# Kernel optimization log

Measured on AMD Instinct MI355X. Metric: run time of the kernel, lower is better.

The kernel has to match this reference:

```python
import jax, jax.numpy as jnp
import numpy as np

N = 100000
E = 1600000
D_IN = 128
D_HID = 128
D_OUT = 64


def mish(x):
    return x * jnp.tanh(jax.nn.softplus(x))


def sage_conv(x, src, dst, W_l, b_l, W_r):
    # gather source-node features along edges, mean-aggregate at destination
    msg = x[src]  # [E, d]
    agg = jax.ops.segment_sum(msg, dst, num_segments=N)  # [N, d]
    cnt = jax.ops.segment_sum(jnp.ones((E,), x.dtype), dst, num_segments=N)
    agg = agg / jnp.maximum(cnt, 1.0)[:, None]
    # PyG SAGEConv: lin_l(aggregated) + lin_r(root); lin_r has no bias
    return agg @ W_l.T + b_l + x @ W_r.T


def setup_inputs() -> dict:
    key = jax.random.key(0)
    ks = jax.random.split(key, 10)
    s = lambda d: 1.0 / np.sqrt(d)
    return {
        "x": jax.random.normal(ks[0], (N, D_IN), jnp.float32),
        "edge_index": jax.random.randint(ks[1], (2, E), 0, N, jnp.int64),
        "W_l0": jax.random.normal(ks[2], (D_HID, D_IN), jnp.float32) * s(D_IN),
        "b_l0": jnp.zeros((D_HID,), jnp.float32),
        "W_r0": jax.random.normal(ks[3], (D_HID, D_IN), jnp.float32) * s(D_IN),
        "W_l1": jax.random.normal(ks[4], (D_HID, D_HID), jnp.float32) * s(D_HID),
        "b_l1": jnp.zeros((D_HID,), jnp.float32),
        "W_r1": jax.random.normal(ks[5], (D_HID, D_HID), jnp.float32) * s(D_HID),
        "W_head": jax.random.normal(ks[6], (D_OUT, D_HID), jnp.float32) * s(D_HID),
        "b_head": jnp.zeros((D_OUT,), jnp.float32),
    }


def reference(x, edge_index, W_l0, b_l0, W_r0, W_l1, b_l1, W_r1, W_head, b_head):
    src, dst = edge_index[0], edge_index[1]
    h = mish(sage_conv(x, src, dst, W_l0, b_l0, W_r0))  # dropout is identity in eval
    h = mish(sage_conv(h, src, dst, W_l1, b_l1, W_r1))
    return h @ W_head.T + b_head
```

## Files before the change

### kernel.cpp

```cpp
#include <hip/hip_runtime.h>
#include <math.h>

#define N_NODES 100000
#define N_EDGES 1600000
#define DF      128
#define D_HEAD  64

#define NWIN    128
#define WIN_SZ  782
#define CAP     13312
#define BCH     8192

typedef __attribute__((ext_vector_type(8))) short bf16x8;
typedef __attribute__((ext_vector_type(4))) float f32x4;

static __device__ __forceinline__ float mish_f(float v) {
    float e = __expf(v);
    float q = 1.0f + e;
    float p = q * q;
    float m = v * (p - 1.0f) / (p + 1.0f);
    return (v > 40.0f) ? v : m;
}

static __device__ __forceinline__ unsigned short f2bf(float f) {
    unsigned int u = __builtin_bit_cast(unsigned int, f);
    unsigned int r = (u + 0x7fffu + ((u >> 16) & 1u)) >> 16;
    return (unsigned short)r;
}


#define XB 12500
#define WB 288

__global__ void cvt_kernel(const float* __restrict__ x,
                           const float* __restrict__ Wl0, const float* __restrict__ Wr0,
                           const float* __restrict__ Wl1, const float* __restrict__ Wr1,
                           const float* __restrict__ Wh,
                           unsigned short* __restrict__ xb, unsigned short* __restrict__ wb,
                           int* __restrict__ bucket_cnt) {
    int b = blockIdx.x;
    if (b < XB) {
        int i = b * 256 + threadIdx.x;
        float4 v = ((const float4*)x)[i];
        ushort4 o;
        o.x = f2bf(v.x); o.y = f2bf(v.y); o.z = f2bf(v.z); o.w = f2bf(v.w);
        ((ushort4*)xb)[i] = o;
    } else if (b < XB + WB) {
        int id = (b - XB) * 256 + threadIdx.x;
        if (id < 65536) {
            int seg = id >> 14;
            int r   = id & 16383;
            const float* W = (seg == 0) ? Wl0 : (seg == 1) ? Wr0 : (seg == 2) ? Wl1 : Wr1;
            wb[id] = f2bf(W[r]);
        } else {
            wb[id] = f2bf(Wh[id - 65536]);
        }
    } else {
        if (threadIdx.x < NWIN) bucket_cnt[threadIdx.x] = 0;
    }
}


__global__ __launch_bounds__(256) void bucket_kernel(const int* __restrict__ src,
                                                     const int* __restrict__ dst,
                                                     int* __restrict__ bucket_cnt,
                                                     unsigned int* __restrict__ pairs) {
    __shared__ int cnt[NWIN][4];
    __shared__ int cur[NWIN][4];
    int tid = threadIdx.x;
    int set = tid & 3;
    int e0  = blockIdx.x * BCH;
    for (int i = tid; i < NWIN * 4; i += 256) ((int*)cnt)[i] = 0;
    __syncthreads();

    int dc[BCH / 256];
    #pragma unroll 4
    for (int i = 0; i < BCH / 256; ++i) {
        int e = e0 + tid + i * 256;
        int d = (e < N_EDGES) ? dst[e] : -1;
        dc[i] = d;
        if (d >= 0) atomicAdd(&cnt[d / WIN_SZ][set], 1);
    }
    __syncthreads();
    if (tid < NWIN) {
        int c0 = cnt[tid][0], c1 = cnt[tid][1], c2 = cnt[tid][2], c3 = cnt[tid][3];
        int b = atomicAdd(&bucket_cnt[tid], c0 + c1 + c2 + c3);
        cur[tid][0] = b;
        cur[tid][1] = b + c0;
        cur[tid][2] = b + c0 + c1;
        cur[tid][3] = b + c0 + c1 + c2;
    }
    __syncthreads();
    #pragma unroll 4
    for (int i = 0; i < BCH / 256; ++i) {
        int d = dc[i];
        if (d >= 0) {
            int e  = e0 + tid + i * 256;
            int s  = src[e];
            int w  = d / WIN_SZ;
            int dl = d - w * WIN_SZ;
            int idx = atomicAdd(&cur[w][set], 1);
            if (idx < CAP)
                pairs[(size_t)w * CAP + idx] = (unsigned)s | ((unsigned)dl << 17);
        }
    }
}


__global__ __launch_bounds__(256) void build_win(const unsigned int* __restrict__ pairs,
                                                 const int* __restrict__ bucket_cnt,
                                                 int* __restrict__ rowstart,
                                                 int* __restrict__ csr) {
    __shared__ int ldeg[WIN_SZ];
    __shared__ int lcsr[CAP];
    __shared__ int wsum[4];
    __shared__ int red[4];

    int tid = threadIdx.x;
    int w   = blockIdx.x;
    int base_node = w * WIN_SZ;
    int nn = N_NODES - base_node;
    if (nn > WIN_SZ) nn = WIN_SZ;
    if (nn < 0) nn = 0;

    for (int i = tid; i < WIN_SZ; i += 256) ldeg[i] = 0;

    int val = (tid < w) ? bucket_cnt[tid] : 0;
    #pragma unroll
    for (int o = 32; o; o >>= 1) val += __shfl_xor(val, o);
    if ((tid & 63) == 0) red[tid >> 6] = val;
    int n_pairs = bucket_cnt[w];
    if (n_pairs > CAP) n_pairs = CAP;
    __syncthreads();
    int ebase = red[0] + red[1] + red[2] + red[3];

    const unsigned int* pw = pairs + (size_t)w * CAP;

    for (int i = tid; i < n_pairs; i += 256)
        atomicAdd(&ldeg[pw[i] >> 17], 1);
    __syncthreads();

    int i0 = tid * 4;
    int v[4];
    int s = 0;
    #pragma unroll
    for (int q = 0; q < 4; ++q) {
        v[q] = (i0 + q < nn) ? ldeg[i0 + q] : 0;
        s += v[q];
    }
    int lane = tid & 63, wv = tid >> 6;
    int sc = s;
    #pragma unroll
    for (int d = 1; d < 64; d <<= 1) {
        int t = __shfl_up(sc, d);
        if (lane >= d) sc += t;
    }
    if (lane == 63) wsum[wv] = sc;
    __syncthreads();
    int woff = 0;
    for (int q = 0; q < wv; ++q) woff += wsum[q];
    int run = woff + sc - s;
    #pragma unroll
    for (int q = 0; q < 4; ++q) {
        if (i0 + q < nn) {
            rowstart[base_node + i0 + q] = ebase + run;
            ldeg[i0 + q] = run;
            run += v[q];
        }
    }
    if (w == NWIN - 1 && tid == 0) rowstart[N_NODES] = N_EDGES;
    __syncthreads();

    for (int i = tid; i < n_pairs; i += 256) {
        unsigned int p = pw[i];
        int slot = atomicAdd(&ldeg[p >> 17], 1);
        lcsr[slot] = (int)(p & 0x1FFFFu);
    }
    __syncthreads();

    for (int i = tid; i < n_pairs; i += 256)
        csr[ebase + i] = lcsr[i];
}


__global__ __launch_bounds__(256) void aggregate_kernel(const unsigned short* __restrict__ X,
                                                        const int* __restrict__ rowstart,
                                                        const int* __restrict__ csr,
                                                        unsigned short* __restrict__ out) {
    int wv   = threadIdx.x >> 6;
    int lane = threadIdx.x & 63;
    int node = blockIdx.x * 4 + wv;
    if (node >= N_NODES) return;
    int slot = lane >> 4;
    int l16  = lane & 15;
    int rs0 = rowstart[node];
    int rs1 = rowstart[node + 1];

    float acc[8];
    #pragma unroll
    for (int i = 0; i < 8; ++i) acc[i] = 0.f;

    for (int e0 = rs0; e0 < rs1; e0 += 16) {
        uint4 v[4];
        #pragma unroll
        for (int j = 0; j < 4; ++j) {
            int e = e0 + 4 * j + slot;
            uint4 t = {0u, 0u, 0u, 0u};
            if (e < rs1) t = *(const uint4*)(X + (size_t)csr[e] * DF + l16 * 8);
            v[j] = t;
        }
        #pragma unroll
        for (int j = 0; j < 4; ++j) {
            unsigned int w0[4] = {v[j].x, v[j].y, v[j].z, v[j].w};
            #pragma unroll
            for (int i = 0; i < 4; ++i) {
                acc[2 * i]     += __builtin_bit_cast(float, w0[i] << 16);
                acc[2 * i + 1] += __builtin_bit_cast(float, w0[i] & 0xffff0000u);
            }
        }
    }

    #pragma unroll
    for (int i = 0; i < 8; ++i) {
        acc[i] += __shfl_xor(acc[i], 32);
        acc[i] += __shfl_xor(acc[i], 16);
    }

    int d = rs1 - rs0;
    float inv = 1.0f / (float)(d > 0 ? d : 1);
    if (slot == 0) {
        unsigned int r[4];
        #pragma unroll
        for (int i = 0; i < 4; ++i) {
            unsigned int lo = f2bf(acc[2 * i] * inv);
            unsigned int hi = f2bf(acc[2 * i + 1] * inv);
            r[i] = lo | (hi << 16);
        }
        uint4 o = {r[0], r[1], r[2], r[3]};
        *(uint4*)(out + (size_t)node * DF + l16 * 8) = o;
    }
}


template <int COLS, bool TWO, bool MISH, bool OUT_BF16>
__global__ __launch_bounds__(256, 3) void sage_gemm(const unsigned short* __restrict__ A,
                                                    const unsigned short* __restrict__ H,
                                                    const unsigned short* __restrict__ Wl,
                                                    const unsigned short* __restrict__ Wr,
                                                    const float* __restrict__ bias,
                                                    void* __restrict__ out) {
    constexpr int NT  = COLS / 16;
    constexpr int LDA = 136;
    __shared__ unsigned short Ws[COLS * LDA];

    int tid  = threadIdx.x;
    int wv   = tid >> 6;
    int lane = tid & 63;
    int quad = lane >> 4;
    int l16  = lane & 15;
    int m0   = blockIdx.x * 128;

    int arow0 = m0 + wv * 32 + l16;
    int arow1 = arow0 + 16;
    if (arow0 > N_NODES - 1) arow0 = N_NODES - 1;
    if (arow1 > N_NODES - 1) arow1 = N_NODES - 1;

    f32x4 acc[2][NT];
    #pragma unroll
    for (int t = 0; t < 2; ++t)
        #pragma unroll
        for (int n = 0; n < NT; ++n) acc[t][n] = (f32x4){0.f, 0.f, 0.f, 0.f};

    #pragma unroll
    for (int phase = 0; phase < (TWO ? 2 : 1); ++phase) {
        const unsigned short* Ain = phase ? H : A;
        const unsigned short* Win = phase ? Wr : Wl;
        if (phase) __syncthreads();
        #pragma unroll
        for (int i = 0; i < COLS / 16; ++i) {
            int idx = tid + i * 256;
            int r   = idx >> 4;
            int cb  = (idx & 15) * 8;
            *(uint4*)&Ws[r * LDA + cb] = *(const uint4*)&Win[r * 128 + cb];
        }
        __syncthreads();

        const unsigned short* Ap0 = Ain + (size_t)arow0 * 128 + quad * 8;
        const unsigned short* Ap1 = Ain + (size_t)arow1 * 128 + quad * 8;
        #pragma unroll
        for (int ks = 0; ks < 4; ++ks) {
            bf16x8 af0 = *(const bf16x8*)(Ap0 + ks * 32);
            bf16x8 af1 = *(const bf16x8*)(Ap1 + ks * 32);
            #pragma unroll
            for (int n = 0; n < NT; ++n) {
                bf16x8 bfr = *(const bf16x8*)&Ws[(n * 16 + l16) * LDA + ks * 32 + quad * 8];
                acc[0][n] = __builtin_amdgcn_mfma_f32_16x16x32_bf16(af0, bfr, acc[0][n], 0, 0, 0);
                acc[1][n] = __builtin_amdgcn_mfma_f32_16x16x32_bf16(af1, bfr, acc[1][n], 0, 0, 0);
            }
        }
    }

    #pragma unroll
    for (int t = 0; t < 2; ++t) {
        #pragma unroll
        for (int n = 0; n < NT; ++n) {
            int col = n * 16 + l16;
            float b = bias[col];
            #pragma unroll
            for (int r = 0; r < 4; ++r) {
                int row = m0 + wv * 32 + t * 16 + quad * 4 + r;
                if (row < N_NODES) {
                    float v = acc[t][n][r] + b;
                    if constexpr (MISH) v = mish_f(v);
                    if constexpr (OUT_BF16)
                        ((unsigned short*)out)[(size_t)row * COLS + col] = f2bf(v);
                    else
                        ((float*)out)[(size_t)row * COLS + col] = v;
                }
            }
        }
    }
}


extern "C" void kernel_launch(void* const* d_in, const int* in_sizes, int n_in,
                              void* d_out, int out_size, void* d_ws, size_t ws_size,
                              hipStream_t stream) {
    const float* x   = (const float*)d_in[0];
    const int*   ei  = (const int*)d_in[1];
    const float* Wl0 = (const float*)d_in[2];
    const float* bl0 = (const float*)d_in[3];
    const float* Wr0 = (const float*)d_in[4];
    const float* Wl1 = (const float*)d_in[5];
    const float* bl1 = (const float*)d_in[6];
    const float* Wr1 = (const float*)d_in[7];
    const float* Wh  = (const float*)d_in[8];
    const float* bh  = (const float*)d_in[9];
    float* out = (float*)d_out;

    const int* src = ei;
    const int* dst = ei + N_EDGES;

    char* ws = (char*)d_ws;
    size_t off = 0;
    auto alloc = [&](size_t bytes) -> void* {
        void* p = ws + off;
        off += (bytes + 255) & ~(size_t)255;
        return p;
    };
    int* rowstart   = (int*)alloc((N_NODES + 1) * 4);
    int* csr        = (int*)alloc(N_EDGES * 4);
    int* bucket_cnt = (int*)alloc(NWIN * 4);

    unsigned short* Wb  = (unsigned short*)alloc((size_t)(65536 + 8192) * 2);
    unsigned short* Xb  = (unsigned short*)alloc((size_t)N_NODES * DF * 2);
    unsigned short* Ab  = (unsigned short*)alloc((size_t)N_NODES * DF * 2);
    unsigned short* H1b = (unsigned short*)alloc((size_t)N_NODES * DF * 2);

    unsigned short* Wlb0 = Wb;
    unsigned short* Wrb0 = Wb + 16384;
    unsigned short* Wlb1 = Wb + 32768;
    unsigned short* Wrb1 = Wb + 49152;
    unsigned short* Whb  = Wb + 65536;
    unsigned short* H2b  = Xb;
    unsigned int* pairs  = (unsigned int*)H1b;

    cvt_kernel<<<XB + WB + 1, 256, 0, stream>>>(x, Wl0, Wr0, Wl1, Wr1, Wh, Xb, Wb, bucket_cnt);

    bucket_kernel<<<(N_EDGES + BCH - 1) / BCH, 256, 0, stream>>>(src, dst, bucket_cnt, pairs);
    build_win<<<NWIN, 256, 0, stream>>>(pairs, bucket_cnt, rowstart, csr);

    const int grid = (N_NODES + 127) / 128;

    aggregate_kernel<<<N_NODES / 4, 256, 0, stream>>>(Xb, rowstart, csr, Ab);
    sage_gemm<128, true, true, true><<<grid, 256, 0, stream>>>(Ab, Xb, Wlb0, Wrb0, bl0, H1b);
    aggregate_kernel<<<N_NODES / 4, 256, 0, stream>>>(H1b, rowstart, csr, Ab);
    sage_gemm<128, true, true, true><<<grid, 256, 0, stream>>>(Ab, H1b, Wlb1, Wrb1, bl1, H2b);
    sage_gemm<64, false, false, false><<<grid, 256, 0, stream>>>(H2b, nullptr, Whb, nullptr, bh, out);
}
```

Measured before the change: 356.9 us.

## Fuse layer-2 GEMM with head, merge convert and bucketing, double window count

The layer-2 SAGE GEMM and the output head GEMM become one kernel: the mish-activated hidden tile is stored as bf16 in shared memory and fed straight into the head MFMA, so the H2 round trip through global memory and one launch are removed. The conversion and edge-bucketing kernels are merged into a single launch, with a tiny separate kernel zeroing the counters. The window count doubles (256 windows of 391 nodes) so more blocks share the CSR build. Risks are an extra launch for zeroing, a smaller per-window capacity that could overflow on skewed graphs, and the head weights being read from global memory inside the fused kernel.

New measurement: 334.4 us. -6.3%, faster.

```diff
diff --git a/kernel.cpp b/kernel.cpp
--- a/kernel.cpp
+++ b/kernel.cpp
@@ -6,10 +6,11 @@
 #define DF      128
 #define D_HEAD  64
 
-#define NWIN    128
-#define WIN_SZ  782
-#define CAP     13312
+#define NWIN    256
+#define WIN_SZ  391
+#define CAP     6912
 #define BCH     8192
+#define NBUCK   ((N_EDGES + BCH - 1) / BCH)
 
 typedef __attribute__((ext_vector_type(8))) short bf16x8;
 typedef __attribute__((ext_vector_type(4))) float f32x4;
@@ -29,47 +30,51 @@
 }
 
 
+__global__ void zero_cnt_kernel(int* __restrict__ bucket_cnt) {
+    bucket_cnt[threadIdx.x] = 0;
+}
+
+
 #define XB 12500
 #define WB 288
 
-__global__ void cvt_kernel(const float* __restrict__ x,
-                           const float* __restrict__ Wl0, const float* __restrict__ Wr0,
-                           const float* __restrict__ Wl1, const float* __restrict__ Wr1,
-                           const float* __restrict__ Wh,
-                           unsigned short* __restrict__ xb, unsigned short* __restrict__ wb,
-                           int* __restrict__ bucket_cnt) {
-    int b = blockIdx.x;
-    if (b < XB) {
-        int i = b * 256 + threadIdx.x;
-        float4 v = ((const float4*)x)[i];
-        ushort4 o;
-        o.x = f2bf(v.x); o.y = f2bf(v.y); o.z = f2bf(v.z); o.w = f2bf(v.w);
-        ((ushort4*)xb)[i] = o;
-    } else if (b < XB + WB) {
-        int id = (b - XB) * 256 + threadIdx.x;
-        if (id < 65536) {
-            int seg = id >> 14;
-            int r   = id & 16383;
-            const float* W = (seg == 0) ? Wl0 : (seg == 1) ? Wr0 : (seg == 2) ? Wl1 : Wr1;
-            wb[id] = f2bf(W[r]);
-        } else {
-            wb[id] = f2bf(Wh[id - 65536]);
-        }
-    } else {
-        if (threadIdx.x < NWIN) bucket_cnt[threadIdx.x] = 0;
-    }
-}
-
-
-__global__ __launch_bounds__(256) void bucket_kernel(const int* __restrict__ src,
-                                                     const int* __restrict__ dst,
-                                                     int* __restrict__ bucket_cnt,
-                                                     unsigned int* __restrict__ pairs) {
+__global__ __launch_bounds__(256) void cvt_bucket_kernel(
+        const float* __restrict__ x,
+        const float* __restrict__ Wl0, const float* __restrict__ Wr0,
+        const float* __restrict__ Wl1, const float* __restrict__ Wr1,
+        const float* __restrict__ Wh,
+        const int* __restrict__ src, const int* __restrict__ dst,
+        unsigned short* __restrict__ xb, unsigned short* __restrict__ wb,
+        int* __restrict__ bucket_cnt, unsigned int* __restrict__ pairs) {
     __shared__ int cnt[NWIN][4];
     __shared__ int cur[NWIN][4];
+    int b   = blockIdx.x;
     int tid = threadIdx.x;
+
+    if (b >= NBUCK) {
+        int cb = b - NBUCK;
+        if (cb < XB) {
+            int i = cb * 256 + tid;
+            float4 v = ((const float4*)x)[i];
+            ushort4 o;
+            o.x = f2bf(v.x); o.y = f2bf(v.y); o.z = f2bf(v.z); o.w = f2bf(v.w);
+            ((ushort4*)xb)[i] = o;
+        } else {
+            int id = (cb - XB) * 256 + tid;
+            if (id < 65536) {
+                int seg = id >> 14;
+                int r   = id & 16383;
+                const float* W = (seg == 0) ? Wl0 : (seg == 1) ? Wr0 : (seg == 2) ? Wl1 : Wr1;
+                wb[id] = f2bf(W[r]);
+            } else {
+                wb[id] = f2bf(Wh[id - 65536]);
+            }
+        }
+        return;
+    }
+
     int set = tid & 3;
-    int e0  = blockIdx.x * BCH;
+    int e0  = b * BCH;
     for (int i = tid; i < NWIN * 4; i += 256) ((int*)cnt)[i] = 0;
     __syncthreads();
 
@@ -82,13 +87,13 @@
         if (d >= 0) atomicAdd(&cnt[d / WIN_SZ][set], 1);
     }
     __syncthreads();
-    if (tid < NWIN) {
-        int c0 = cnt[tid][0], c1 = cnt[tid][1], c2 = cnt[tid][2], c3 = cnt[tid][3];
-        int b = atomicAdd(&bucket_cnt[tid], c0 + c1 + c2 + c3);
-        cur[tid][0] = b;
-        cur[tid][1] = b + c0;
-        cur[tid][2] = b + c0 + c1;
-        cur[tid][3] = b + c0 + c1 + c2;
+    for (int w = tid; w < NWIN; w += 256) {
+        int c0 = cnt[w][0], c1 = cnt[w][1], c2 = cnt[w][2], c3 = cnt[w][3];
+        int base = atomicAdd(&bucket_cnt[w], c0 + c1 + c2 + c3);
+        cur[w][0] = base;
+        cur[w][1] = base + c0;
+        cur[w][2] = base + c0 + c1;
+        cur[w][3] = base + c0 + c1 + c2;
     }
     __syncthreads();
     #pragma unroll 4
@@ -140,11 +145,11 @@
         atomicAdd(&ldeg[pw[i] >> 17], 1);
     __syncthreads();
 
-    int i0 = tid * 4;
-    int v[4];
+    int i0 = tid * 2;
+    int v[2];
     int s = 0;
     #pragma unroll
-    for (int q = 0; q < 4; ++q) {
+    for (int q = 0; q < 2; ++q) {
         v[q] = (i0 + q < nn) ? ldeg[i0 + q] : 0;
         s += v[q];
     }
@@ -161,7 +166,7 @@
     for (int q = 0; q < wv; ++q) woff += wsum[q];
     int run = woff + sc - s;
     #pragma unroll
-    for (int q = 0; q < 4; ++q) {
+    for (int q = 0; q < 2; ++q) {
         if (i0 + q < nn) {
             rowstart[base_node + i0 + q] = ebase + run;
             ldeg[i0 + q] = run;
@@ -317,6 +322,116 @@
                     else
                         ((float*)out)[(size_t)row * COLS + col] = v;
                 }
+            }
+        }
+    }
+}
+
+
+__global__ __launch_bounds__(256, 3) void sage_gemm1_head(const unsigned short* __restrict__ A,
+                                                          const unsigned short* __restrict__ H,
+                                                          const unsigned short* __restrict__ Wl,
+                                                          const unsigned short* __restrict__ Wr,
+                                                          const float* __restrict__ bias,
+                                                          const unsigned short* __restrict__ Wh,
+                                                          const float* __restrict__ bh,
+                                                          float* __restrict__ out) {
+    constexpr int LDA = 136;
+    __shared__ unsigned short Ws[128 * LDA];
+
+    int tid  = threadIdx.x;
+    int wv   = tid >> 6;
+    int lane = tid & 63;
+    int quad = lane >> 4;
+    int l16  = lane & 15;
+    int m0   = blockIdx.x * 128;
+
+    int arow0 = m0 + wv * 32 + l16;
+    int arow1 = arow0 + 16;
+    if (arow0 > N_NODES - 1) arow0 = N_NODES - 1;
+    if (arow1 > N_NODES - 1) arow1 = N_NODES - 1;
+
+    f32x4 acc0[2][8];
+    #pragma unroll
+    for (int t = 0; t < 2; ++t)
+        #pragma unroll
+        for (int n = 0; n < 8; ++n) acc0[t][n] = (f32x4){0.f, 0.f, 0.f, 0.f};
+
+    #pragma unroll
+    for (int phase = 0; phase < 2; ++phase) {
+        const unsigned short* Ain = phase ? H : A;
+        const unsigned short* Win = phase ? Wr : Wl;
+        if (phase) __syncthreads();
+        #pragma unroll
+        for (int i = 0; i < 8; ++i) {
+            int idx = tid + i * 256;
+            int r   = idx >> 4;
+            int cb  = (idx & 15) * 8;
+            *(uint4*)&Ws[r * LDA + cb] = *(const uint4*)&Win[r * 128 + cb];
+        }
+        __syncthreads();
+
+        const unsigned short* Ap0 = Ain + (size_t)arow0 * 128 + quad * 8;
+        const unsigned short* Ap1 = Ain + (size_t)arow1 * 128 + quad * 8;
+        #pragma unroll
+        for (int ks = 0; ks < 4; ++ks) {
+            bf16x8 af0 = *(const bf16x8*)(Ap0 + ks * 32);
+            bf16x8 af1 = *(const bf16x8*)(Ap1 + ks * 32);
+            #pragma unroll
+            for (int n = 0; n < 8; ++n) {
+                bf16x8 bfr = *(const bf16x8*)&Ws[(n * 16 + l16) * LDA + ks * 32 + quad * 8];
+                acc0[0][n] = __builtin_amdgcn_mfma_f32_16x16x32_bf16(af0, bfr, acc0[0][n], 0, 0, 0);
+                acc0[1][n] = __builtin_amdgcn_mfma_f32_16x16x32_bf16(af1, bfr, acc0[1][n], 0, 0, 0);
+            }
+        }
+    }
+    __syncthreads();
+
+    #pragma unroll
+    for (int t = 0; t < 2; ++t) {
+        #pragma unroll
+        for (int n = 0; n < 8; ++n) {
+            int col = n * 16 + l16;
+            float b = bias[col];
+            #pragma unroll
+            for (int r = 0; r < 4; ++r) {
+                int row = wv * 32 + t * 16 + quad * 4 + r;
+                Ws[row * LDA + col] = f2bf(mish_f(acc0[t][n][r] + b));
+            }
+        }
+    }
+    __syncthreads();
+
+    f32x4 acc2[2][4];
+    #pragma unroll
+    for (int t = 0; t < 2; ++t)
+        #pragma unroll
+        for (int n = 0; n < 4; ++n) acc2[t][n] = (f32x4){0.f, 0.f, 0.f, 0.f};
+
+    int ar0 = wv * 32 + l16;
+    #pragma unroll
+    for (int ks = 0; ks < 4; ++ks) {
+        bf16x8 af0 = *(const bf16x8*)&Ws[ar0 * LDA + ks * 32 + quad * 8];
+        bf16x8 af1 = *(const bf16x8*)&Ws[(ar0 + 16) * LDA + ks * 32 + quad * 8];
+        #pragma unroll
+        for (int n = 0; n < 4; ++n) {
+            bf16x8 bfr = *(const bf16x8*)&Wh[(n * 16 + l16) * 128 + ks * 32 + quad * 8];
+            acc2[0][n] = __builtin_amdgcn_mfma_f32_16x16x32_bf16(af0, bfr, acc2[0][n], 0, 0, 0);
+            acc2[1][n] = __builtin_amdgcn_mfma_f32_16x16x32_bf16(af1, bfr, acc2[1][n], 0, 0, 0);
+        }
+    }
+
+    #pragma unroll
+    for (int t = 0; t < 2; ++t) {
+        #pragma unroll
+        for (int n = 0; n < 4; ++n) {
+            int col = n * 16 + l16;
+            float b = bh[col];
+            #pragma unroll
+            for (int r = 0; r < 4; ++r) {
+                int row = m0 + wv * 32 + t * 16 + quad * 4 + r;
+                if (row < N_NODES)
+                    out[(size_t)row * D_HEAD + col] = acc2[t][n][r] + b;
             }
         }
     }
@@ -362,12 +477,13 @@
     unsigned short* Wlb1 = Wb + 32768;
     unsigned short* Wrb1 = Wb + 49152;
     unsigned short* Whb  = Wb + 65536;
-    unsigned short* H2b  = Xb;
     unsigned int* pairs  = (unsigned int*)H1b;
 
-    cvt_kernel<<<XB + WB + 1, 256, 0, stream>>>(x, Wl0, Wr0, Wl1, Wr1, Wh, Xb, Wb, bucket_cnt);
-
-    bucket_kernel<<<(N_EDGES + BCH - 1) / BCH, 256, 0, stream>>>(src, dst, bucket_cnt, pairs);
+    zero_cnt_kernel<<<1, NWIN, 0, stream>>>(bucket_cnt);
+
+    cvt_bucket_kernel<<<NBUCK + XB + WB, 256, 0, stream>>>(
+        x, Wl0, Wr0, Wl1, Wr1, Wh, src, dst, Xb, Wb, bucket_cnt, pairs);
+
     build_win<<<NWIN, 256, 0, stream>>>(pairs, bucket_cnt, rowstart, csr);
 
     const int grid = (N_NODES + 127) / 128;
@@ -375,6 +491,5 @@
     aggregate_kernel<<<N_NODES / 4, 256, 0, stream>>>(Xb, rowstart, csr, Ab);
     sage_gemm<128, true, true, true><<<grid, 256, 0, stream>>>(Ab, Xb, Wlb0, Wrb0, bl0, H1b);
     aggregate_kernel<<<N_NODES / 4, 256, 0, stream>>>(H1b, rowstart, csr, Ab);
-    sage_gemm<128, true, true, true><<<grid, 256, 0, stream>>>(Ab, H1b, Wlb1, Wrb1, bl1, H2b);
-    sage_gemm<64, false, false, false><<<grid, 256, 0, stream>>>(H2b, nullptr, Whb, nullptr, bh, out);
-}
+    sage_gemm1_head<<<grid, 256, 0, stream>>>(Ab, H1b, Wlb1, Wrb1, bl1, Whb, bh, out);
+}
```
